# Optimization experiments

Hardware: AMD Instinct MI355X
Metric: run time of the kernel (lower is better)

The kernel has to match this reference:

```python
import jax, jax.numpy as jnp
import numpy as np

N_NODES = 50000
N_GRAPHS = 50
MAX_NODES = 1000  # equal-size graphs
C_IN = 128
C_OUT = 128
N_EDGES = 800000
N_LAYERS = 3
BN_EPS = 1e-5


def setup_inputs() -> dict:
    key = jax.random.key(0)
    ks = jax.random.split(key, 20)
    x = jax.random.normal(ks[0], (N_NODES, C_IN), dtype=jnp.float32)
    edge_index = jax.random.randint(ks[1], (2, N_EDGES), 0, N_NODES, dtype=jnp.int64)
    batch = jnp.repeat(jnp.arange(N_GRAPHS, dtype=jnp.int64), MAX_NODES)
    s_in = 1.0 / np.sqrt(C_IN)
    s_out = 1.0 / np.sqrt(C_OUT)
    fh_W = jax.random.normal(ks[2], (C_IN, C_OUT), dtype=jnp.float32) * s_in
    fh_b = jnp.zeros((C_OUT,), dtype=jnp.float32)
    W1 = jax.random.normal(ks[3], (N_LAYERS, C_OUT, C_OUT), dtype=jnp.float32) * s_out
    b1 = jnp.zeros((N_LAYERS, C_OUT), dtype=jnp.float32)
    g1 = jnp.ones((N_LAYERS, C_OUT), dtype=jnp.float32)
    be1 = jnp.zeros((N_LAYERS, C_OUT), dtype=jnp.float32)
    W2 = jax.random.normal(ks[4], (N_LAYERS, C_OUT, C_OUT), dtype=jnp.float32) * s_out
    b2 = jnp.zeros((N_LAYERS, C_OUT), dtype=jnp.float32)
    g2 = jnp.ones((N_LAYERS, C_OUT), dtype=jnp.float32)
    be2 = jnp.zeros((N_LAYERS, C_OUT), dtype=jnp.float32)
    return {"x": x, "edge_index": edge_index, "batch": batch,
            "fh_W": fh_W, "fh_b": fh_b,
            "W1": W1, "b1": b1, "g1": g1, "be1": be1,
            "W2": W2, "b2": b2, "g2": g2, "be2": be2}


def _bn(h, gamma, beta):
    # training-mode BatchNorm1d over the node dim (biased variance, like torch)
    mu = jnp.mean(h, axis=0)
    var = jnp.var(h, axis=0)
    return (h - mu) * jax.lax.rsqrt(var + BN_EPS) * gamma + beta


def _mlp(h, W1, b1, g1, be1, W2, b2, g2, be2):
    h = jax.nn.relu(_bn(h @ W1 + b1, g1, be1))
    h = jax.nn.relu(_bn(h @ W2 + b2, g2, be2))
    return h


def _to_dense_batch(h, batch):
    # counts per graph -> exclusive starts -> intra-graph position
    ones = jnp.ones((h.shape[0],), dtype=jnp.int32)
    counts = jax.ops.segment_sum(ones, batch, num_segments=N_GRAPHS)
    starts = jnp.cumsum(counts) - counts
    pos = jnp.arange(h.shape[0], dtype=jnp.int32) - starts[batch]
    dense = jnp.zeros((N_GRAPHS, MAX_NODES, h.shape[1]), dtype=h.dtype)
    return dense.at[batch, pos].set(h)


def reference(x, edge_index, batch, fh_W, fh_b, W1, b1, g1, be1, W2, b2, g2, be2):
    src, dst = edge_index[0], edge_index[1]
    h = x @ fh_W + fh_b  # first_head Linear
    outs = [_to_dense_batch(h, batch)]
    for l in range(N_LAYERS):
        # GINConv: mlp((1+eps)*x + sum_{j->i} x_j), eps=0
        agg = jax.ops.segment_sum(h[src], dst, num_segments=N_NODES)
        h = _mlp(h + agg, W1[l], b1[l], g1[l], be1[l], W2[l], b2[l], g2[l], be2[l])
        outs.append(_to_dense_batch(h, batch))
    return jnp.stack(outs)  # [N_LAYERS+1, B, MAX_NODES, C]
```

## Files before the change

kernel.cpp:

```cpp
#include <hip/hip_runtime.h>

#define NN 50000
#define NE 800000
#define CC 128
#define SLAB (NN * CC)
#define BN_EPS 1e-5f

typedef __attribute__((ext_vector_type(8))) short bf16x8;
typedef __attribute__((ext_vector_type(4))) float f32x4;
typedef unsigned short ushort_t;

__device__ inline ushort_t f2bf(float v) {
  unsigned u = __builtin_bit_cast(unsigned, v);
  unsigned r = u + 0x7FFFu + ((u >> 16) & 1u);
  return (ushort_t)(r >> 16);
}
__device__ inline float bf2f(unsigned hi16_lo) {
  return __builtin_bit_cast(float, hi16_lo << 16);
}

__global__ void zero_int_kernel(int* __restrict__ p, int n) {
  int i = blockIdx.x * blockDim.x + threadIdx.x;
  if (i < n) p[i] = 0;
}

__global__ void count_kernel(const int* __restrict__ dst, int* __restrict__ counts) {
  int e = blockIdx.x * blockDim.x + threadIdx.x;
  if (e < NE) atomicAdd(&counts[dst[e]], 1);
}

__global__ void scan1_kernel(const int* __restrict__ counts, int* __restrict__ excl,
                             int* __restrict__ blocksum) {
  __shared__ int s[256];
  int t = threadIdx.x;
  int i = blockIdx.x * 256 + t;
  int v = (i < NN) ? counts[i] : 0;
  s[t] = v;
  for (int off = 1; off < 256; off <<= 1) {
    __syncthreads();
    int add = (t >= off) ? s[t - off] : 0;
    __syncthreads();
    s[t] += add;
  }
  __syncthreads();
  if (i < NN) excl[i] = s[t] - v;
  if (t == 255) blocksum[blockIdx.x] = s[255];
}

__global__ void scan2_kernel(int* __restrict__ blocksum, int nb) {
  __shared__ int s[256];
  int t = threadIdx.x;
  int v = (t < nb) ? blocksum[t] : 0;
  s[t] = v;
  for (int off = 1; off < 256; off <<= 1) {
    __syncthreads();
    int add = (t >= off) ? s[t - off] : 0;
    __syncthreads();
    s[t] += add;
  }
  __syncthreads();
  if (t < nb) blocksum[t] = s[t] - v;
}

__global__ void scan3_kernel(int* __restrict__ excl, const int* __restrict__ blocksum) {
  int i = blockIdx.x * 256 + threadIdx.x;
  if (i < NN) excl[i] += blocksum[blockIdx.x];
}

__global__ void fill_kernel(const int* __restrict__ src, const int* __restrict__ dst,
                            const int* __restrict__ starts, int* __restrict__ fill,
                            int* __restrict__ bucket) {
  int e = blockIdx.x * blockDim.x + threadIdx.x;
  if (e < NE) {
    int d = dst[e];
    int pos = atomicAdd(&fill[d], 1);
    bucket[starts[d] + pos] = src[e];
  }
}

__global__ void prep_w_kernel(const float* __restrict__ fh_W, const float* __restrict__ W1,
                              const float* __restrict__ W2, short* __restrict__ whi,
                              short* __restrict__ wlo) {
  int m = blockIdx.x;
  const float* src = (m == 0) ? fh_W : ((m <= 3) ? W1 + (m - 1) * CC * CC : W2 + (m - 4) * CC * CC);
  short* hi = whi + m * CC * CC;
  short* lo = wlo + m * CC * CC;
  for (int it = 0; it < 64; ++it) {
    int idx = it * 256 + threadIdx.x;
    int j = idx & 7;
    int l = (idx >> 3) & 63;
    int nt = (idx >> 9) & 7;
    int ks = idx >> 12;
    int n = nt * 16 + (l & 15);
    int k = ks * 32 + ((l >> 4) << 3) + j;
    float v = src[k * CC + n];
    unsigned u = __builtin_bit_cast(unsigned, v);
    unsigned short h = (unsigned short)(u >> 16);
    float hf = __builtin_bit_cast(float, ((unsigned)h) << 16);
    float r = v - hf;
    unsigned ur = __builtin_bit_cast(unsigned, r);
    hi[idx] = (short)h;
    lo[idx] = (short)(ur >> 16);
  }
}

__global__ __launch_bounds__(256) void gemm0_kernel(
    const float* __restrict__ A, const short* __restrict__ Wp_hi, const short* __restrict__ Wp_lo,
    const float* __restrict__ bias, float* __restrict__ out, ushort_t* __restrict__ h16) {
  const int t = threadIdx.x;
  const int l = t & 63;
  const int wv = t >> 6;
  const int m0 = blockIdx.x * 64 + wv * 16;
  const int row = m0 + (l & 15);
  const int kg = (l >> 4) * 8;

  f32x4 acc[8];
#pragma unroll
  for (int i = 0; i < 8; ++i) acc[i] = (f32x4){0.f, 0.f, 0.f, 0.f};

#pragma unroll
  for (int ks = 0; ks < 4; ++ks) {
    float av[8];
    if (row < NN) {
      const float* ap = &A[row * CC + ks * 32 + kg];
      float4 v0 = *(const float4*)ap;
      float4 v1 = *(const float4*)(ap + 4);
      av[0] = v0.x; av[1] = v0.y; av[2] = v0.z; av[3] = v0.w;
      av[4] = v1.x; av[5] = v1.y; av[6] = v1.z; av[7] = v1.w;
    } else {
#pragma unroll
      for (int i = 0; i < 8; ++i) av[i] = 0.f;
    }
    bf16x8 ah, al;
#pragma unroll
    for (int i = 0; i < 8; ++i) {
      unsigned u = __builtin_bit_cast(unsigned, av[i]);
      unsigned short hbits = (unsigned short)(u >> 16);
      float hf = __builtin_bit_cast(float, ((unsigned)hbits) << 16);
      float r = av[i] - hf;
      unsigned ur = __builtin_bit_cast(unsigned, r);
      ah[i] = (short)hbits;
      al[i] = (short)(ur >> 16);
    }
#pragma unroll
    for (int nt = 0; nt < 8; ++nt) {
      const int base = (ks * 8 + nt) * 512 + l * 8;
      bf16x8 wh = *(const bf16x8*)&Wp_hi[base];
      bf16x8 wl = *(const bf16x8*)&Wp_lo[base];
      acc[nt] = __builtin_amdgcn_mfma_f32_16x16x32_bf16(ah, wh, acc[nt], 0, 0, 0);
      acc[nt] = __builtin_amdgcn_mfma_f32_16x16x32_bf16(al, wh, acc[nt], 0, 0, 0);
      acc[nt] = __builtin_amdgcn_mfma_f32_16x16x32_bf16(ah, wl, acc[nt], 0, 0, 0);
    }
  }

  const int rbase = m0 + (l >> 4) * 4;
  const int cn = l & 15;
#pragma unroll
  for (int nt = 0; nt < 8; ++nt) {
    int c = nt * 16 + cn;
    float bv = bias[c];
#pragma unroll
    for (int r = 0; r < 4; ++r) {
      int rr = rbase + r;
      if (rr < NN) {
        float v = acc[nt][r] + bv;
        out[rr * CC + c] = v;
        h16[rr * CC + c] = f2bf(v);
      }
    }
  }
}

__global__ __launch_bounds__(256) void fused1_kernel(
    const ushort_t* __restrict__ h16, const int* __restrict__ starts,
    const int* __restrict__ counts, const int* __restrict__ bucket,
    const short* __restrict__ Wp_hi, const short* __restrict__ Wp_lo,
    const float* __restrict__ bias, ushort_t* __restrict__ tmp16,
    float* __restrict__ stats_out) {
  __shared__ ushort_t tile[4][16][128];
  __shared__ float sred[2 * CC];
  const int t = threadIdx.x;
  const int l = t & 63;
  const int wv = t >> 6;
  const int q = l >> 4;
  const int j16 = l & 15;
  const int m0 = blockIdx.x * 64 + wv * 16;
  sred[t] = 0.f;

  const uint4* tbl = (const uint4*)h16;

  for (int j = 0; j < 16; ++j) {
    const int node = m0 + j;
    float acc[8];
#pragma unroll
    for (int k = 0; k < 8; ++k) acc[k] = 0.f;
    if (node < NN) {
      if (q == 0) {
        uint4 u = tbl[node * 16 + j16];
        acc[0] = bf2f(u.x & 0xFFFF); acc[1] = bf2f(u.x >> 16);
        acc[2] = bf2f(u.y & 0xFFFF); acc[3] = bf2f(u.y >> 16);
        acc[4] = bf2f(u.z & 0xFFFF); acc[5] = bf2f(u.z >> 16);
        acc[6] = bf2f(u.w & 0xFFFF); acc[7] = bf2f(u.w >> 16);
      }
      const int s = starts[node];
      const int n = counts[node];
      for (int base = 0; base < n; base += 64) {
        int nb = min(n - base, 64);
        int idx = (l < nb) ? bucket[s + base + l] : 0;
        int jj = 0;
        for (; jj + 16 <= nb; jj += 16) {
          int sr0 = __shfl(idx, jj + q);
          int sr1 = __shfl(idx, jj + 4 + q);
          int sr2 = __shfl(idx, jj + 8 + q);
          int sr3 = __shfl(idx, jj + 12 + q);
          uint4 a = tbl[sr0 * 16 + j16];
          uint4 b = tbl[sr1 * 16 + j16];
          uint4 cc2 = tbl[sr2 * 16 + j16];
          uint4 d = tbl[sr3 * 16 + j16];
          acc[0] += bf2f(a.x & 0xFFFF) + bf2f(b.x & 0xFFFF) + bf2f(cc2.x & 0xFFFF) + bf2f(d.x & 0xFFFF);
          acc[1] += bf2f(a.x >> 16) + bf2f(b.x >> 16) + bf2f(cc2.x >> 16) + bf2f(d.x >> 16);
          acc[2] += bf2f(a.y & 0xFFFF) + bf2f(b.y & 0xFFFF) + bf2f(cc2.y & 0xFFFF) + bf2f(d.y & 0xFFFF);
          acc[3] += bf2f(a.y >> 16) + bf2f(b.y >> 16) + bf2f(cc2.y >> 16) + bf2f(d.y >> 16);
          acc[4] += bf2f(a.z & 0xFFFF) + bf2f(b.z & 0xFFFF) + bf2f(cc2.z & 0xFFFF) + bf2f(d.z & 0xFFFF);
          acc[5] += bf2f(a.z >> 16) + bf2f(b.z >> 16) + bf2f(cc2.z >> 16) + bf2f(d.z >> 16);
          acc[6] += bf2f(a.w & 0xFFFF) + bf2f(b.w & 0xFFFF) + bf2f(cc2.w & 0xFFFF) + bf2f(d.w & 0xFFFF);
          acc[7] += bf2f(a.w >> 16) + bf2f(b.w >> 16) + bf2f(cc2.w >> 16) + bf2f(d.w >> 16);
        }
        for (; jj < nb; jj += 4) {
          int i = jj + q;
          int sr = __shfl(idx, (i < nb) ? i : (nb - 1));
          if (i < nb) {
            uint4 a = tbl[sr * 16 + j16];
            acc[0] += bf2f(a.x & 0xFFFF); acc[1] += bf2f(a.x >> 16);
            acc[2] += bf2f(a.y & 0xFFFF); acc[3] += bf2f(a.y >> 16);
            acc[4] += bf2f(a.z & 0xFFFF); acc[5] += bf2f(a.z >> 16);
            acc[6] += bf2f(a.w & 0xFFFF); acc[7] += bf2f(a.w >> 16);
          }
        }
      }
#pragma unroll
      for (int k = 0; k < 8; ++k) {
        acc[k] += __shfl_xor(acc[k], 16);
        acc[k] += __shfl_xor(acc[k], 32);
      }
    }
    if (q == 0) {
      uint4 o;
      o.x = (unsigned)f2bf(acc[0]) | ((unsigned)f2bf(acc[1]) << 16);
      o.y = (unsigned)f2bf(acc[2]) | ((unsigned)f2bf(acc[3]) << 16);
      o.z = (unsigned)f2bf(acc[4]) | ((unsigned)f2bf(acc[5]) << 16);
      o.w = (unsigned)f2bf(acc[6]) | ((unsigned)f2bf(acc[7]) << 16);
      int byteoff = (j16 * 16) ^ ((j & 7) << 4);
      *(uint4*)((char*)&tile[wv][j][0] + byteoff) = o;
    }
  }
  __syncthreads();

  f32x4 acc2[8];
#pragma unroll
  for (int i = 0; i < 8; ++i) acc2[i] = (f32x4){0.f, 0.f, 0.f, 0.f};

#pragma unroll
  for (int ks = 0; ks < 4; ++ks) {
    int byteoff = ((ks * 4 + q) * 16) ^ ((j16 & 7) << 4);
    bf16x8 ah = *(const bf16x8*)((const char*)&tile[wv][j16][0] + byteoff);
#pragma unroll
    for (int nt = 0; nt < 8; ++nt) {
      const int base = (ks * 8 + nt) * 512 + l * 8;
      bf16x8 wh = *(const bf16x8*)&Wp_hi[base];
      bf16x8 wl = *(const bf16x8*)&Wp_lo[base];
      acc2[nt] = __builtin_amdgcn_mfma_f32_16x16x32_bf16(ah, wh, acc2[nt], 0, 0, 0);
      acc2[nt] = __builtin_amdgcn_mfma_f32_16x16x32_bf16(ah, wl, acc2[nt], 0, 0, 0);
    }
  }

  const int rbase = m0 + (l >> 4) * 4;
  const int cn = l & 15;
#pragma unroll
  for (int nt = 0; nt < 8; ++nt) {
    int c = nt * 16 + cn;
    float bv = bias[c];
    float s = 0.f, qq = 0.f;
#pragma unroll
    for (int r = 0; r < 4; ++r) {
      int rr = rbase + r;
      if (rr < NN) {
        float v = acc2[nt][r] + bv;
        tmp16[rr * CC + c] = f2bf(v);
        s += v; qq += v * v;
      }
    }
    s += __shfl_xor(s, 16); s += __shfl_xor(s, 32);
    qq += __shfl_xor(qq, 16); qq += __shfl_xor(qq, 32);
    if (q == 0) {
      atomicAdd(&sred[c], s);
      atomicAdd(&sred[CC + c], qq);
    }
  }
  __syncthreads();
  atomicAdd(&stats_out[t], sred[t]);
}

__global__ __launch_bounds__(256) void gemm2_kernel(
    const ushort_t* __restrict__ tmp16, const short* __restrict__ Wp_hi,
    const short* __restrict__ Wp_lo, const float* __restrict__ bias,
    const float* __restrict__ stats_in, const float* __restrict__ g,
    const float* __restrict__ be, float* __restrict__ tmp2, float* __restrict__ stats_out) {
  __shared__ float sred[2 * CC];
  const int t = threadIdx.x;
  const int l = t & 63;
  const int wv = t >> 6;
  const int m0 = blockIdx.x * 64 + wv * 16;
  const int row = m0 + (l & 15);
  const int kg = (l >> 4) * 8;
  sred[t] = 0.f;

  f32x4 acc[8];
#pragma unroll
  for (int i = 0; i < 8; ++i) acc[i] = (f32x4){0.f, 0.f, 0.f, 0.f};

#pragma unroll
  for (int ks = 0; ks < 4; ++ks) {
    bf16x8 ah;
    if (row < NN) {
      bf16x8 raw = *(const bf16x8*)&tmp16[row * CC + ks * 32 + kg];
#pragma unroll
      for (int i = 0; i < 8; ++i) {
        int c = ks * 32 + kg + i;
        float mu = stats_in[c] * (1.0f / NN);
        float var = fmaxf(stats_in[CC + c] * (1.0f / NN) - mu * mu, 0.f);
        float a = g[c] * rsqrtf(var + BN_EPS);
        float d = fmaf(-mu, a, be[c]);
        float v = bf2f((unsigned)(ushort_t)raw[i]);
        v = fmaxf(fmaf(v, a, d), 0.f);
        ah[i] = (short)f2bf(v);
      }
    } else {
#pragma unroll
      for (int i = 0; i < 8; ++i) ah[i] = 0;
    }
#pragma unroll
    for (int nt = 0; nt < 8; ++nt) {
      const int base = (ks * 8 + nt) * 512 + l * 8;
      bf16x8 wh = *(const bf16x8*)&Wp_hi[base];
      bf16x8 wl = *(const bf16x8*)&Wp_lo[base];
      acc[nt] = __builtin_amdgcn_mfma_f32_16x16x32_bf16(ah, wh, acc[nt], 0, 0, 0);
      acc[nt] = __builtin_amdgcn_mfma_f32_16x16x32_bf16(ah, wl, acc[nt], 0, 0, 0);
    }
  }

  __syncthreads();
  const int rbase = m0 + (l >> 4) * 4;
  const int cn = l & 15;
#pragma unroll
  for (int nt = 0; nt < 8; ++nt) {
    int c = nt * 16 + cn;
    float bv = bias[c];
    float s = 0.f, qq = 0.f;
#pragma unroll
    for (int r = 0; r < 4; ++r) {
      int rr = rbase + r;
      if (rr < NN) {
        float v = acc[nt][r] + bv;
        tmp2[rr * CC + c] = v;
        s += v; qq += v * v;
      }
    }
    s += __shfl_xor(s, 16); s += __shfl_xor(s, 32);
    qq += __shfl_xor(qq, 16); qq += __shfl_xor(qq, 32);
    if ((l >> 4) == 0) {
      atomicAdd(&sred[c], s);
      atomicAdd(&sred[CC + c], qq);
    }
  }
  __syncthreads();
  atomicAdd(&stats_out[t], sred[t]);
}

__global__ void apply_kernel(const float* __restrict__ tmp, const float* __restrict__ stats2,
                             const float* __restrict__ g2, const float* __restrict__ be2,
                             float* __restrict__ outslab, ushort_t* __restrict__ h16) {
  int i = blockIdx.x * blockDim.x + threadIdx.x;
  float4 v = ((const float4*)tmp)[i];
  int c = (i & 31) << 2;
  float4 sm = *(const float4*)&stats2[c];
  float4 sq = *(const float4*)&stats2[CC + c];
  float4 gg = *(const float4*)&g2[c];
  float4 bb = *(const float4*)&be2[c];
  float4 a, d;
  {
    float mu = sm.x * (1.0f / NN), var = fmaxf(sq.x * (1.0f / NN) - mu * mu, 0.f);
    a.x = gg.x * rsqrtf(var + BN_EPS); d.x = fmaf(-mu, a.x, bb.x);
    mu = sm.y * (1.0f / NN); var = fmaxf(sq.y * (1.0f / NN) - mu * mu, 0.f);
    a.y = gg.y * rsqrtf(var + BN_EPS); d.y = fmaf(-mu, a.y, bb.y);
    mu = sm.z * (1.0f / NN); var = fmaxf(sq.z * (1.0f / NN) - mu * mu, 0.f);
    a.z = gg.z * rsqrtf(var + BN_EPS); d.z = fmaf(-mu, a.z, bb.z);
    mu = sm.w * (1.0f / NN); var = fmaxf(sq.w * (1.0f / NN) - mu * mu, 0.f);
    a.w = gg.w * rsqrtf(var + BN_EPS); d.w = fmaf(-mu, a.w, bb.w);
  }
  v.x = fmaxf(fmaf(v.x, a.x, d.x), 0.f);
  v.y = fmaxf(fmaf(v.y, a.y, d.y), 0.f);
  v.z = fmaxf(fmaf(v.z, a.z, d.z), 0.f);
  v.w = fmaxf(fmaf(v.w, a.w, d.w), 0.f);
  ((float4*)outslab)[i] = v;
  if (h16) {
    ushort_t p[4] = {f2bf(v.x), f2bf(v.y), f2bf(v.z), f2bf(v.w)};
    *(uint2*)&h16[i * 4] = *(uint2*)p;
  }
}

extern "C" void kernel_launch(void* const* d_in, const int* in_sizes, int n_in,
                              void* d_out, int out_size, void* d_ws, size_t ws_size,
                              hipStream_t stream) {
  const float* x    = (const float*)d_in[0];
  const int*   edge = (const int*)d_in[1];
  const float* fh_W = (const float*)d_in[3];
  const float* fh_b = (const float*)d_in[4];
  const float* W1   = (const float*)d_in[5];
  const float* b1   = (const float*)d_in[6];
  const float* g1   = (const float*)d_in[7];
  const float* be1  = (const float*)d_in[8];
  const float* W2   = (const float*)d_in[9];
  const float* b2   = (const float*)d_in[10];
  const float* g2   = (const float*)d_in[11];
  const float* be2  = (const float*)d_in[12];
  float* out = (float*)d_out;

  const int* src = edge;
  const int* dst = edge + NE;

  int* counts   = (int*)d_ws;
  int* fill     = counts + 50048;
  float* stats  = (float*)(fill + 50048);
  int* starts   = (int*)(stats + 1536);
  int* blocksum = starts + 50048;
  int* bucket   = blocksum + 256;
  short* whi    = (short*)(bucket + NE);
  short* wlo    = whi + 7 * CC * CC;
  ushort_t* h16 = (ushort_t*)(wlo + 7 * CC * CC);
  ushort_t* tmp16 = h16 + SLAB;
  float* tmp2   = (float*)(tmp16 + SLAB);

  zero_int_kernel<<<(101632 + 255) / 256, 256, 0, stream>>>(counts, 101632);
  count_kernel<<<NE / 256, 256, 0, stream>>>(dst, counts);
  scan1_kernel<<<196, 256, 0, stream>>>(counts, starts, blocksum);
  scan2_kernel<<<1, 256, 0, stream>>>(blocksum, 196);
  scan3_kernel<<<196, 256, 0, stream>>>(starts, blocksum);
  fill_kernel<<<NE / 256, 256, 0, stream>>>(src, dst, starts, fill, bucket);

  prep_w_kernel<<<7, 256, 0, stream>>>(fh_W, W1, W2, whi, wlo);

  gemm0_kernel<<<782, 256, 0, stream>>>(x, whi, wlo, fh_b, out, h16);

  for (int ly = 0; ly < 3; ++ly) {
    float* stats1 = stats + (ly * 2) * 256;
    float* stats2 = stats + (ly * 2 + 1) * 256;
    fused1_kernel<<<782, 256, 0, stream>>>(
        h16, starts, counts, bucket, whi + (1 + ly) * CC * CC, wlo + (1 + ly) * CC * CC,
        b1 + ly * CC, tmp16, stats1);
    gemm2_kernel<<<782, 256, 0, stream>>>(
        tmp16, whi + (4 + ly) * CC * CC, wlo + (4 + ly) * CC * CC, b2 + ly * CC,
        stats1, g1 + ly * CC, be1 + ly * CC, tmp2, stats2);
    apply_kernel<<<SLAB / 4 / 256, 256, 0, stream>>>(
        tmp2, stats2, g2 + ly * CC, be2 + ly * CC, out + (ly + 1) * SLAB,
        (ly < 2) ? h16 : (ushort_t*)nullptr);
  }
}
```

Baseline: 497.8 us.

## Slice node features into channel-major bf16 blocks and split gather from GEMM

Activations are now stored in a sliced bf16 layout: 8 slices of 16 channels, each slice contiguous over nodes. The edge-gather aggregation becomes its own kernel, launched with one block per 16 nodes per slice, which writes a sliced aggregate buffer. A separate gemm1 kernel reads that buffer as its MFMA A operand. The intent is a smaller per-slice gather working set that sits better in cache, plus a simpler GEMM that no longer serializes behind the gather. The second GEMM's output changes from fp32 to bf16, written in place over its input, and the apply kernel is reworked to read bf16 and emit the sliced layout. Costs include an extra global round trip for the aggregates, narrow 4-byte gather loads, and lower precision before BatchNorm.

```diff
diff --git a/kernel.cpp b/kernel.cpp
--- a/kernel.cpp
+++ b/kernel.cpp
@@ -9,15 +9,14 @@
 typedef __attribute__((ext_vector_type(8))) short bf16x8;
 typedef __attribute__((ext_vector_type(4))) float f32x4;
 typedef unsigned short ushort_t;
+typedef unsigned int uint_t;
 
 __device__ inline ushort_t f2bf(float v) {
   unsigned u = __builtin_bit_cast(unsigned, v);
   unsigned r = u + 0x7FFFu + ((u >> 16) & 1u);
   return (ushort_t)(r >> 16);
 }
-__device__ inline float bf2f(unsigned hi16_lo) {
-  return __builtin_bit_cast(float, hi16_lo << 16);
-}
+__device__ inline float bf2f(unsigned lo16) { return __builtin_bit_cast(float, lo16 << 16); }
 
 __global__ void zero_int_kernel(int* __restrict__ p, int n) {
   int i = blockIdx.x * blockDim.x + threadIdx.x;
@@ -106,7 +105,7 @@
 
 __global__ __launch_bounds__(256) void gemm0_kernel(
     const float* __restrict__ A, const short* __restrict__ Wp_hi, const short* __restrict__ Wp_lo,
-    const float* __restrict__ bias, float* __restrict__ out, ushort_t* __restrict__ h16) {
+    const float* __restrict__ bias, float* __restrict__ out, ushort_t* __restrict__ h16s) {
   const int t = threadIdx.x;
   const int l = t & 63;
   const int wv = t >> 6;
@@ -165,115 +164,94 @@
       if (rr < NN) {
         float v = acc[nt][r] + bv;
         out[rr * CC + c] = v;
-        h16[rr * CC + c] = f2bf(v);
+        h16s[(nt * NN + rr) * 16 + cn] = f2bf(v);
       }
     }
   }
 }
 
-__global__ __launch_bounds__(256) void fused1_kernel(
-    const ushort_t* __restrict__ h16, const int* __restrict__ starts,
+__global__ __launch_bounds__(256) void gather_kernel(
+    const ushort_t* __restrict__ h16s, const int* __restrict__ starts,
     const int* __restrict__ counts, const int* __restrict__ bucket,
-    const short* __restrict__ Wp_hi, const short* __restrict__ Wp_lo,
-    const float* __restrict__ bias, ushort_t* __restrict__ tmp16,
-    float* __restrict__ stats_out) {
-  __shared__ ushort_t tile[4][16][128];
+    ushort_t* __restrict__ aggs) {
+  const int slice = blockIdx.x & 7;
+  const int t = threadIdx.x;
+  const int g16 = t >> 4;
+  const int lane16 = t & 15;
+  const int j8 = lane16 & 7;
+  const int half = lane16 >> 3;
+  const int node = (blockIdx.x >> 3) * 16 + g16;
+  const int wl_base = t & 48;
+  const uint_t* tbl = (const uint_t*)h16s + slice * (NN * 8);
+
+  float a0 = 0.f, a1 = 0.f;
+  if (half == 0) {
+    uint_t u = tbl[node * 8 + j8];
+    a0 = bf2f(u & 0xFFFFu);
+    a1 = bf2f(u >> 16);
+  }
+  const int s = starts[node];
+  const int n = counts[node];
+  for (int base = 0; base < n; base += 16) {
+    int nb = n - base;
+    if (nb > 16) nb = 16;
+    int idx = (lane16 < nb) ? bucket[s + base + lane16] : -1;
+#pragma unroll
+    for (int k = 0; k < 8; ++k) {
+      int sr = __shfl(idx, wl_base + 2 * k + half);
+      if (sr >= 0) {
+        uint_t u = tbl[sr * 8 + j8];
+        a0 += bf2f(u & 0xFFFFu);
+        a1 += bf2f(u >> 16);
+      }
+    }
+  }
+  a0 += __shfl_xor(a0, 8);
+  a1 += __shfl_xor(a1, 8);
+  if (half == 0) {
+    ((uint_t*)aggs)[slice * (NN * 8) + node * 8 + j8] =
+        (uint_t)f2bf(a0) | ((uint_t)f2bf(a1) << 16);
+  }
+}
+
+__global__ __launch_bounds__(256) void gemm1_kernel(
+    const ushort_t* __restrict__ aggs, const short* __restrict__ Wp_hi,
+    const short* __restrict__ Wp_lo, const float* __restrict__ bias,
+    ushort_t* __restrict__ tmp16, float* __restrict__ stats_out) {
   __shared__ float sred[2 * CC];
   const int t = threadIdx.x;
   const int l = t & 63;
   const int wv = t >> 6;
-  const int q = l >> 4;
-  const int j16 = l & 15;
   const int m0 = blockIdx.x * 64 + wv * 16;
+  const int row = m0 + (l & 15);
+  const int kg = (l >> 4) * 8;
   sred[t] = 0.f;
 
-  const uint4* tbl = (const uint4*)h16;
-
-  for (int j = 0; j < 16; ++j) {
-    const int node = m0 + j;
-    float acc[8];
-#pragma unroll
-    for (int k = 0; k < 8; ++k) acc[k] = 0.f;
-    if (node < NN) {
-      if (q == 0) {
-        uint4 u = tbl[node * 16 + j16];
-        acc[0] = bf2f(u.x & 0xFFFF); acc[1] = bf2f(u.x >> 16);
-        acc[2] = bf2f(u.y & 0xFFFF); acc[3] = bf2f(u.y >> 16);
-        acc[4] = bf2f(u.z & 0xFFFF); acc[5] = bf2f(u.z >> 16);
-        acc[6] = bf2f(u.w & 0xFFFF); acc[7] = bf2f(u.w >> 16);
-      }
-      const int s = starts[node];
-      const int n = counts[node];
-      for (int base = 0; base < n; base += 64) {
-        int nb = min(n - base, 64);
-        int idx = (l < nb) ? bucket[s + base + l] : 0;
-        int jj = 0;
-        for (; jj + 16 <= nb; jj += 16) {
-          int sr0 = __shfl(idx, jj + q);
-          int sr1 = __shfl(idx, jj + 4 + q);
-          int sr2 = __shfl(idx, jj + 8 + q);
-          int sr3 = __shfl(idx, jj + 12 + q);
-          uint4 a = tbl[sr0 * 16 + j16];
-          uint4 b = tbl[sr1 * 16 + j16];
-          uint4 cc2 = tbl[sr2 * 16 + j16];
-          uint4 d = tbl[sr3 * 16 + j16];
-          acc[0] += bf2f(a.x & 0xFFFF) + bf2f(b.x & 0xFFFF) + bf2f(cc2.x & 0xFFFF) + bf2f(d.x & 0xFFFF);
-          acc[1] += bf2f(a.x >> 16) + bf2f(b.x >> 16) + bf2f(cc2.x >> 16) + bf2f(d.x >> 16);
-          acc[2] += bf2f(a.y & 0xFFFF) + bf2f(b.y & 0xFFFF) + bf2f(cc2.y & 0xFFFF) + bf2f(d.y & 0xFFFF);
-          acc[3] += bf2f(a.y >> 16) + bf2f(b.y >> 16) + bf2f(cc2.y >> 16) + bf2f(d.y >> 16);
-          acc[4] += bf2f(a.z & 0xFFFF) + bf2f(b.z & 0xFFFF) + bf2f(cc2.z & 0xFFFF) + bf2f(d.z & 0xFFFF);
-          acc[5] += bf2f(a.z >> 16) + bf2f(b.z >> 16) + bf2f(cc2.z >> 16) + bf2f(d.z >> 16);
-          acc[6] += bf2f(a.w & 0xFFFF) + bf2f(b.w & 0xFFFF) + bf2f(cc2.w & 0xFFFF) + bf2f(d.w & 0xFFFF);
-          acc[7] += bf2f(a.w >> 16) + bf2f(b.w >> 16) + bf2f(cc2.w >> 16) + bf2f(d.w >> 16);
-        }
-        for (; jj < nb; jj += 4) {
-          int i = jj + q;
-          int sr = __shfl(idx, (i < nb) ? i : (nb - 1));
-          if (i < nb) {
-            uint4 a = tbl[sr * 16 + j16];
-            acc[0] += bf2f(a.x & 0xFFFF); acc[1] += bf2f(a.x >> 16);
-            acc[2] += bf2f(a.y & 0xFFFF); acc[3] += bf2f(a.y >> 16);
-            acc[4] += bf2f(a.z & 0xFFFF); acc[5] += bf2f(a.z >> 16);
-            acc[6] += bf2f(a.w & 0xFFFF); acc[7] += bf2f(a.w >> 16);
-          }
-        }
-      }
-#pragma unroll
-      for (int k = 0; k < 8; ++k) {
-        acc[k] += __shfl_xor(acc[k], 16);
-        acc[k] += __shfl_xor(acc[k], 32);
-      }
-    }
-    if (q == 0) {
-      uint4 o;
-      o.x = (unsigned)f2bf(acc[0]) | ((unsigned)f2bf(acc[1]) << 16);
-      o.y = (unsigned)f2bf(acc[2]) | ((unsigned)f2bf(acc[3]) << 16);
-      o.z = (unsigned)f2bf(acc[4]) | ((unsigned)f2bf(acc[5]) << 16);
-      o.w = (unsigned)f2bf(acc[6]) | ((unsigned)f2bf(acc[7]) << 16);
-      int byteoff = (j16 * 16) ^ ((j & 7) << 4);
-      *(uint4*)((char*)&tile[wv][j][0] + byteoff) = o;
-    }
-  }
-  __syncthreads();
-
-  f32x4 acc2[8];
-#pragma unroll
-  for (int i = 0; i < 8; ++i) acc2[i] = (f32x4){0.f, 0.f, 0.f, 0.f};
+  f32x4 acc[8];
+#pragma unroll
+  for (int i = 0; i < 8; ++i) acc[i] = (f32x4){0.f, 0.f, 0.f, 0.f};
 
 #pragma unroll
   for (int ks = 0; ks < 4; ++ks) {
-    int byteoff = ((ks * 4 + q) * 16) ^ ((j16 & 7) << 4);
-    bf16x8 ah = *(const bf16x8*)((const char*)&tile[wv][j16][0] + byteoff);
+    const int ch0 = ks * 32 + kg;
+    bf16x8 ah;
+    if (row < NN) {
+      ah = *(const bf16x8*)&aggs[((ch0 >> 4) * NN + row) * 16 + (ch0 & 15)];
+    } else {
+#pragma unroll
+      for (int i = 0; i < 8; ++i) ah[i] = 0;
+    }
 #pragma unroll
     for (int nt = 0; nt < 8; ++nt) {
       const int base = (ks * 8 + nt) * 512 + l * 8;
       bf16x8 wh = *(const bf16x8*)&Wp_hi[base];
       bf16x8 wl = *(const bf16x8*)&Wp_lo[base];
-      acc2[nt] = __builtin_amdgcn_mfma_f32_16x16x32_bf16(ah, wh, acc2[nt], 0, 0, 0);
-      acc2[nt] = __builtin_amdgcn_mfma_f32_16x16x32_bf16(ah, wl, acc2[nt], 0, 0, 0);
-    }
-  }
-
+      acc[nt] = __builtin_amdgcn_mfma_f32_16x16x32_bf16(ah, wh, acc[nt], 0, 0, 0);
+      acc[nt] = __builtin_amdgcn_mfma_f32_16x16x32_bf16(ah, wl, acc[nt], 0, 0, 0);
+    }
+  }
+
+  __syncthreads();
   const int rbase = m0 + (l >> 4) * 4;
   const int cn = l & 15;
 #pragma unroll
@@ -285,14 +263,14 @@
     for (int r = 0; r < 4; ++r) {
       int rr = rbase + r;
       if (rr < NN) {
-        float v = acc2[nt][r] + bv;
+        float v = acc[nt][r] + bv;
         tmp16[rr * CC + c] = f2bf(v);
         s += v; qq += v * v;
       }
     }
     s += __shfl_xor(s, 16); s += __shfl_xor(s, 32);
     qq += __shfl_xor(qq, 16); qq += __shfl_xor(qq, 32);
-    if (q == 0) {
+    if ((l >> 4) == 0) {
       atomicAdd(&sred[c], s);
       atomicAdd(&sred[CC + c], qq);
     }
@@ -302,10 +280,10 @@
 }
 
 __global__ __launch_bounds__(256) void gemm2_kernel(
-    const ushort_t* __restrict__ tmp16, const short* __restrict__ Wp_hi,
+    ushort_t* __restrict__ tmp16, const short* __restrict__ Wp_hi,
     const short* __restrict__ Wp_lo, const float* __restrict__ bias,
     const float* __restrict__ stats_in, const float* __restrict__ g,
-    const float* __restrict__ be, float* __restrict__ tmp2, float* __restrict__ stats_out) {
+    const float* __restrict__ be, float* __restrict__ stats_out) {
   __shared__ float sred[2 * CC];
   const int t = threadIdx.x;
   const int l = t & 63;
@@ -362,7 +340,7 @@
       int rr = rbase + r;
       if (rr < NN) {
         float v = acc[nt][r] + bv;
-        tmp2[rr * CC + c] = v;
+        tmp16[rr * CC + c] = f2bf(v);
         s += v; qq += v * v;
       }
     }
@@ -377,35 +355,55 @@
   atomicAdd(&stats_out[t], sred[t]);
 }
 
-__global__ void apply_kernel(const float* __restrict__ tmp, const float* __restrict__ stats2,
-                             const float* __restrict__ g2, const float* __restrict__ be2,
-                             float* __restrict__ outslab, ushort_t* __restrict__ h16) {
-  int i = blockIdx.x * blockDim.x + threadIdx.x;
-  float4 v = ((const float4*)tmp)[i];
-  int c = (i & 31) << 2;
-  float4 sm = *(const float4*)&stats2[c];
-  float4 sq = *(const float4*)&stats2[CC + c];
-  float4 gg = *(const float4*)&g2[c];
-  float4 bb = *(const float4*)&be2[c];
-  float4 a, d;
-  {
-    float mu = sm.x * (1.0f / NN), var = fmaxf(sq.x * (1.0f / NN) - mu * mu, 0.f);
-    a.x = gg.x * rsqrtf(var + BN_EPS); d.x = fmaf(-mu, a.x, bb.x);
-    mu = sm.y * (1.0f / NN); var = fmaxf(sq.y * (1.0f / NN) - mu * mu, 0.f);
-    a.y = gg.y * rsqrtf(var + BN_EPS); d.y = fmaf(-mu, a.y, bb.y);
-    mu = sm.z * (1.0f / NN); var = fmaxf(sq.z * (1.0f / NN) - mu * mu, 0.f);
-    a.z = gg.z * rsqrtf(var + BN_EPS); d.z = fmaf(-mu, a.z, bb.z);
-    mu = sm.w * (1.0f / NN); var = fmaxf(sq.w * (1.0f / NN) - mu * mu, 0.f);
-    a.w = gg.w * rsqrtf(var + BN_EPS); d.w = fmaf(-mu, a.w, bb.w);
-  }
-  v.x = fmaxf(fmaf(v.x, a.x, d.x), 0.f);
-  v.y = fmaxf(fmaf(v.y, a.y, d.y), 0.f);
-  v.z = fmaxf(fmaf(v.z, a.z, d.z), 0.f);
-  v.w = fmaxf(fmaf(v.w, a.w, d.w), 0.f);
-  ((float4*)outslab)[i] = v;
-  if (h16) {
-    ushort_t p[4] = {f2bf(v.x), f2bf(v.y), f2bf(v.z), f2bf(v.w)};
-    *(uint2*)&h16[i * 4] = *(uint2*)p;
+__global__ __launch_bounds__(256) void apply_kernel(
+    const ushort_t* __restrict__ t2, const float* __restrict__ stats2,
+    const float* __restrict__ g2, const float* __restrict__ be2,
+    float* __restrict__ outslab, ushort_t* __restrict__ h16s) {
+  const int node = blockIdx.x * 256 + threadIdx.x;
+  const int slice = blockIdx.y;
+  if (node >= NN) return;
+  const int c0 = slice * 16;
+
+  const uint4* tp = (const uint4*)(t2 + node * CC + c0);
+  uint4 r0 = tp[0], r1 = tp[1];
+  unsigned w[4] = {r0.x, r0.y, r0.z, r0.w};
+  unsigned w2[4] = {r1.x, r1.y, r1.z, r1.w};
+
+  float vo[16];
+#pragma unroll
+  for (int j = 0; j < 8; ++j) {
+    unsigned u = (j < 4) ? w[j] : w2[j - 4];
+    vo[2 * j] = bf2f(u & 0xFFFFu);
+    vo[2 * j + 1] = bf2f(u >> 16);
+  }
+#pragma unroll
+  for (int j = 0; j < 16; ++j) {
+    int c = c0 + j;
+    float mu = stats2[c] * (1.0f / NN);
+    float var = fmaxf(stats2[CC + c] * (1.0f / NN) - mu * mu, 0.f);
+    float a = g2[c] * rsqrtf(var + BN_EPS);
+    float d = fmaf(-mu, a, be2[c]);
+    vo[j] = fmaxf(fmaf(vo[j], a, d), 0.f);
+  }
+  float* op = &outslab[node * CC + c0];
+#pragma unroll
+  for (int j = 0; j < 4; ++j) {
+    float4 v = make_float4(vo[4 * j], vo[4 * j + 1], vo[4 * j + 2], vo[4 * j + 3]);
+    *(float4*)&op[4 * j] = v;
+  }
+  if (h16s) {
+    uint4 o0, o1;
+    o0.x = (unsigned)f2bf(vo[0]) | ((unsigned)f2bf(vo[1]) << 16);
+    o0.y = (unsigned)f2bf(vo[2]) | ((unsigned)f2bf(vo[3]) << 16);
+    o0.z = (unsigned)f2bf(vo[4]) | ((unsigned)f2bf(vo[5]) << 16);
+    o0.w = (unsigned)f2bf(vo[6]) | ((unsigned)f2bf(vo[7]) << 16);
+    o1.x = (unsigned)f2bf(vo[8]) | ((unsigned)f2bf(vo[9]) << 16);
+    o1.y = (unsigned)f2bf(vo[10]) | ((unsigned)f2bf(vo[11]) << 16);
+    o1.z = (unsigned)f2bf(vo[12]) | ((unsigned)f2bf(vo[13]) << 16);
+    o1.w = (unsigned)f2bf(vo[14]) | ((unsigned)f2bf(vo[15]) << 16);
+    uint4* hp = (uint4*)(h16s + (slice * NN + node) * 16);
+    hp[0] = o0;
+    hp[1] = o1;
   }
 }
 
@@ -437,9 +435,9 @@
   int* bucket   = blocksum + 256;
   short* whi    = (short*)(bucket + NE);
   short* wlo    = whi + 7 * CC * CC;
-  ushort_t* h16 = (ushort_t*)(wlo + 7 * CC * CC);
-  ushort_t* tmp16 = h16 + SLAB;
-  float* tmp2   = (float*)(tmp16 + SLAB);
+  ushort_t* h16s = (ushort_t*)(wlo + 7 * CC * CC);
+  ushort_t* aggs = h16s + SLAB;
+  ushort_t* tmp16 = aggs + SLAB;
 
   zero_int_kernel<<<(101632 + 255) / 256, 256, 0, stream>>>(counts, 101632);
   count_kernel<<<NE / 256, 256, 0, stream>>>(dst, counts);
@@ -450,19 +448,19 @@
 
   prep_w_kernel<<<7, 256, 0, stream>>>(fh_W, W1, W2, whi, wlo);
 
-  gemm0_kernel<<<782, 256, 0, stream>>>(x, whi, wlo, fh_b, out, h16);
+  gemm0_kernel<<<782, 256, 0, stream>>>(x, whi, wlo, fh_b, out, h16s);
 
   for (int ly = 0; ly < 3; ++ly) {
     float* stats1 = stats + (ly * 2) * 256;
     float* stats2 = stats + (ly * 2 + 1) * 256;
-    fused1_kernel<<<782, 256, 0, stream>>>(
-        h16, starts, counts, bucket, whi + (1 + ly) * CC * CC, wlo + (1 + ly) * CC * CC,
-        b1 + ly * CC, tmp16, stats1);
+    gather_kernel<<<25000, 256, 0, stream>>>(h16s, starts, counts, bucket, aggs);
+    gemm1_kernel<<<782, 256, 0, stream>>>(
+        aggs, whi + (1 + ly) * CC * CC, wlo + (1 + ly) * CC * CC, b1 + ly * CC, tmp16, stats1);
     gemm2_kernel<<<782, 256, 0, stream>>>(
         tmp16, whi + (4 + ly) * CC * CC, wlo + (4 + ly) * CC * CC, b2 + ly * CC,
-        stats1, g1 + ly * CC, be1 + ly * CC, tmp2, stats2);
-    apply_kernel<<<SLAB / 4 / 256, 256, 0, stream>>>(
-        tmp2, stats2, g2 + ly * CC, be2 + ly * CC, out + (ly + 1) * SLAB,
-        (ly < 2) ? h16 : (ushort_t*)nullptr);
-  }
-}
+        stats1, g1 + ly * CC, be1 + ly * CC, stats2);
+    apply_kernel<<<dim3(196, 8), 256, 0, stream>>>(
+        tmp16, stats2, g2 + ly * CC, be2 + ly * CC, out + (ly + 1) * SLAB,
+        (ly < 2) ? h16s : (ushort_t*)nullptr);
+  }
+}
```

After: 571.8 us. 1.15x slower.
